# Performance work log

Hardware: AMD Instinct MI355X
Metric: run time of the kernel (lower is better)

## Reference

```python
import jax, jax.numpy as jnp
import numpy as np

EPS = 1e-12

def _l2norm(x):
    # F.normalize(p=2, dim=-1) with torch's eps clamp
    n = jnp.sqrt(jnp.sum(x * x, axis=-1, keepdims=True))
    return x / jnp.maximum(n, EPS)

def setup_inputs() -> dict:
    key = jax.random.key(0)
    k1, k2, k3, k4 = jax.random.split(key, 4)
    B, Lq, Ld, H, D = 64, 32, 256, 768, 128
    Q_hidden = jax.random.normal(k1, (B, Lq, H), dtype=jnp.float32)
    D_hidden = jax.random.normal(k2, (B, Ld, H), dtype=jnp.float32)
    W = jax.random.normal(k3, (D, H), dtype=jnp.float32) * (1.0 / np.sqrt(H))
    d_mask = jax.random.randint(k4, (B, Ld), 0, 2).astype(bool)
    d_mask = d_mask.at[:, 0].set(True)  # every doc has >=1 valid token
    return {"Q_hidden": Q_hidden, "D_hidden": D_hidden, "W": W, "d_mask": d_mask}

def reference(Q_hidden, D_hidden, W, d_mask):
    # linear projection (no bias) + L2 normalize, as in query()/doc()
    Q = _l2norm(jnp.einsum('blh,dh->bld', Q_hidden, W))       # [B,Lq,D]
    Dv = _l2norm(jnp.einsum('blh,dh->bld', D_hidden, W))      # [B,Ld,D]
    Dv = Dv * d_mask[..., None].astype(Dv.dtype)              # zero padded/skiplist tokens
    # intra-batch cosine MaxSim: sim[b,c,q,n] = Q[b,q] . D[c,n]
    sim = jnp.einsum('bqd,cnd->bcqn', Q, Dv)                  # [B,B,Lq,Ld]
    sim = jnp.where(d_mask[None, :, None, :], sim, -jnp.inf)  # mask doc tokens
    return jnp.sum(jnp.max(sim, axis=-1), axis=-1)            # [B,B]
```

## Files before the change

kernel.cpp:

```cpp
#include <hip/hip_runtime.h>
#include <hip/hip_bf16.h>
#include <math.h>

typedef __attribute__((ext_vector_type(4))) float f32x4;
typedef __attribute__((ext_vector_type(8))) short bf16x8;

#define NB    64
#define LQ    32
#define LDOC  256
#define HDIM  768
#define DDIM  128
#define NTOK_Q (NB * LQ)
#define NTOK_D (NB * LDOC)
#define NTOK   (NTOK_Q + NTOK_D)

#define WS_OFF_W    0
#define WS_OFF_MASK 196608
#define WS_OFF_QN   212992
#define WS_OFF_DN   737280

__device__ inline short f2bf(float f) {
    unsigned u = __float_as_uint(f);
    u = (u + 0x7fffu + ((u >> 16) & 1u)) >> 16;
    return (short)u;
}

__global__ void prep(const float* __restrict__ W, short* __restrict__ Wbf,
                     const unsigned char* __restrict__ mraw,
                     unsigned short* __restrict__ maskT) {
    if (blockIdx.x < 96) {
        int i = blockIdx.x * 256 + threadIdx.x;
        float4 v = *(const float4*)(W + (size_t)i * 4);
        short4 o;
        o.x = f2bf(v.x); o.y = f2bf(v.y); o.z = f2bf(v.z); o.w = f2bf(v.w);
        *(short4*)(Wbf + (size_t)i * 4) = o;
        return;
    }
    __shared__ int dword_ok_s;
    if (threadIdx.x == 0) dword_ok_s = 1;
    __syncthreads();
    const unsigned* dw = (const unsigned*)mraw;
    int ok = 1;
    for (int i = threadIdx.x; i < 4096; i += 256) {
        unsigned v = dw[i];
        if (!(v == 0u || v == 1u || v == 0x3F800000u)) ok = 0;
    }
    if (!ok) atomicAnd(&dword_ok_s, 0);
    __syncthreads();
    const int isdw = dword_ok_s;
    for (int w = threadIdx.x; w < 1024; w += 256) {
        const int c = w >> 4, lcc = w & 15;
        unsigned bits = 0;
        if (isdw) {
            for (int nt = 0; nt < 16; ++nt)
                bits |= (dw[c * 256 + nt * 16 + lcc] ? 1u : 0u) << nt;
        } else {
            for (int nt = 0; nt < 16; ++nt)
                bits |= (mraw[c * 256 + nt * 16 + lcc] ? 1u : 0u) << nt;
        }
        maskT[w] = (unsigned short)bits;
    }
}

__global__ __launch_bounds__(256)
void proj_norm(const float* __restrict__ Qh, const float* __restrict__ Dh,
               const short* __restrict__ Wbf,
               short* __restrict__ Qn, short* __restrict__ Dn) {
    const int tid  = threadIdx.x;
    const int lane = tid & 63;
    const int wave = tid >> 6;
    const int g    = lane >> 4;
    const int lc   = lane & 15;
    const int wr   = wave >> 1;
    const int wc   = wave & 1;
    const int row0 = blockIdx.x * 32;

    const float* Asrc = (row0 < NTOK_Q) ? Qh + (size_t)row0 * HDIM
                                        : Dh + (size_t)(row0 - NTOK_Q) * HDIM;

    __shared__ alignas(16) short As[2][2048];
    __shared__ alignas(16) short Bs[2][8192];
    __shared__ float norms[2][2][16];

    const int arow = tid >> 3, au = tid & 7;
    const float* aga  = Asrc + (size_t)arow * HDIM + au * 8;
    const int    adst = arow * 64 + (au ^ (arow & 7)) * 8;
    const int n0 = tid >> 3,           u0 = tid & 7;
    const int n1 = (256 + tid) >> 3,   u1 = u0;
    const int n2 = (512 + tid) >> 3,   u2 = u0;
    const int n3 = (768 + tid) >> 3,   u3 = u0;
    const short* bga0 = Wbf + (size_t)n0 * HDIM + u0 * 8;
    const short* bga1 = Wbf + (size_t)n1 * HDIM + u1 * 8;
    const short* bga2 = Wbf + (size_t)n2 * HDIM + u2 * 8;
    const short* bga3 = Wbf + (size_t)n3 * HDIM + u3 * 8;
    const int bd0 = n0 * 64 + (u0 ^ (n0 & 7)) * 8;
    const int bd1 = n1 * 64 + (u1 ^ (n1 & 7)) * 8;
    const int bd2 = n2 * 64 + (u2 ^ (n2 & 7)) * 8;
    const int bd3 = n3 * 64 + (u3 ^ (n3 & 7)) * 8;

    float4 ar0, ar1;
    bf16x8 br0, br1, br2, br3;

    auto LOADS = [&](int t) {
        ar0 = *(const float4*)(aga + t * 64);
        ar1 = *(const float4*)(aga + t * 64 + 4);
        br0 = *(const bf16x8*)(bga0 + t * 64);
        br1 = *(const bf16x8*)(bga1 + t * 64);
        br2 = *(const bf16x8*)(bga2 + t * 64);
        br3 = *(const bf16x8*)(bga3 + t * 64);
    };
    auto WRITES = [&](int buf) {
        bf16x8 av;
        av[0] = f2bf(ar0.x); av[1] = f2bf(ar0.y); av[2] = f2bf(ar0.z); av[3] = f2bf(ar0.w);
        av[4] = f2bf(ar1.x); av[5] = f2bf(ar1.y); av[6] = f2bf(ar1.z); av[7] = f2bf(ar1.w);
        *(bf16x8*)(&As[buf][adst]) = av;
        *(bf16x8*)(&Bs[buf][bd0]) = br0;
        *(bf16x8*)(&Bs[buf][bd1]) = br1;
        *(bf16x8*)(&Bs[buf][bd2]) = br2;
        *(bf16x8*)(&Bs[buf][bd3]) = br3;
    };

    f32x4 acc[4];
#pragma unroll
    for (int nt = 0; nt < 4; ++nt) acc[nt] = (f32x4){0.f, 0.f, 0.f, 0.f};

    LOADS(0);
    WRITES(0);
    __syncthreads();

    for (int t = 0; t < 12; ++t) {
        const int cur = t & 1;
        if (t < 11) LOADS(t + 1);
        __builtin_amdgcn_sched_barrier(0);

        const short* Ab = &As[cur][0];
        const short* Bb = &Bs[cur][0];
#pragma unroll
        for (int ks = 0; ks < 2; ++ks) {
            bf16x8 bfr[4];
#pragma unroll
            for (int nt = 0; nt < 4; ++nt) {
                const int nl = wc * 64 + nt * 16 + lc;
                const int c8 = (ks * 4 + g) ^ (nl & 7);
                bfr[nt] = *(const bf16x8*)(Bb + (size_t)nl * 64 + c8 * 8);
            }
            const int rl = wr * 16 + lc;
            const int ua = (ks * 4 + g) ^ (rl & 7);
            bf16x8 af = *(const bf16x8*)(Ab + (size_t)rl * 64 + ua * 8);
#pragma unroll
            for (int nt = 0; nt < 4; ++nt)
                acc[nt] = __builtin_amdgcn_mfma_f32_16x16x32_bf16(af, bfr[nt], acc[nt], 0, 0, 0);
        }
        if (t < 11) WRITES(cur ^ 1);
        __syncthreads();
    }

    float part[4];
#pragma unroll
    for (int i = 0; i < 4; ++i) {
        float s = 0.f;
#pragma unroll
        for (int nt = 0; nt < 4; ++nt) s += acc[nt][i] * acc[nt][i];
        s += __shfl_xor(s, 1);
        s += __shfl_xor(s, 2);
        s += __shfl_xor(s, 4);
        s += __shfl_xor(s, 8);
        part[i] = s;
    }
    if (lc == 0) {
#pragma unroll
        for (int i = 0; i < 4; ++i) norms[wr][wc][g * 4 + i] = part[i];
    }
    __syncthreads();

    short* Obase = (row0 < NTOK_Q) ? Qn + (size_t)row0 * DDIM
                                   : Dn + (size_t)(row0 - NTOK_Q) * DDIM;
#pragma unroll
    for (int i = 0; i < 4; ++i) {
        const int rloc = g * 4 + i;
        const float tot = norms[wr][0][rloc] + norms[wr][1][rloc];
        const float inv = 1.f / fmaxf(sqrtf(tot), 1e-12f);
        short* dst = Obase + (size_t)(wr * 16 + rloc) * DDIM + wc * 64;
#pragma unroll
        for (int nt = 0; nt < 4; ++nt)
            dst[nt * 16 + lc] = f2bf(acc[nt][i] * inv);
    }
}

__global__ __launch_bounds__(512)
void maxsim(const short* __restrict__ Qn, const short* __restrict__ Dn,
            const unsigned short* __restrict__ maskT, float* __restrict__ out) {
    const int x  = blockIdx.x & 7;
    const int m8 = (blockIdx.x >> 3) & 7;
    const int bg = blockIdx.x >> 6;
    const int c  = x * 8 + m8;

    const int tid  = threadIdx.x;
    const int wave = tid >> 6;
    const int lane = tid & 63;
    const int g = lane >> 4, lc = lane & 15;

    __shared__ alignas(16) short Ds[2][8192];

    const short* dsrc = Dn + (size_t)c * LDOC * DDIM;

    const int r0 = tid >> 4,          v0 = tid & 15;
    const int r1 = (512 + tid) >> 4,  v1 = v0;
    const int dd0 = r0 * DDIM + (v0 ^ (r0 & 15)) * 8;
    const int dd1 = r1 * DDIM + (v1 ^ (r1 & 15)) * 8;
    bf16x8 dr0, dr1;

    auto LOADS = [&](int ch) {
        dr0 = *(const bf16x8*)(dsrc + (size_t)(ch * 64 + r0) * DDIM + v0 * 8);
        dr1 = *(const bf16x8*)(dsrc + (size_t)(ch * 64 + r1) * DDIM + v1 * 8);
    };
    auto WRITES = [&](int buf) {
        *(bf16x8*)(&Ds[buf][dd0]) = dr0;
        *(bf16x8*)(&Ds[buf][dd1]) = dr1;
    };

    LOADS(0);
    WRITES(0);

    bf16x8 qf[2][4];
    const int qrow0 = bg * 256 + wave * 32;
#pragma unroll
    for (int m = 0; m < 2; ++m) {
        const short* qb = Qn + (size_t)(qrow0 + m * 16 + lc) * DDIM;
#pragma unroll
        for (int ks = 0; ks < 4; ++ks)
            qf[m][ks] = *(const bf16x8*)(qb + ks * 32 + g * 8);
    }
    const unsigned mbits = maskT[c * 16 + lc];

    __syncthreads();

    float rmax[2][4];
#pragma unroll
    for (int m = 0; m < 2; ++m)
#pragma unroll
        for (int i = 0; i < 4; ++i) rmax[m][i] = -INFINITY;

    for (int ch = 0; ch < 4; ++ch) {
        const int buf = ch & 1;
        if (ch < 3) LOADS(ch + 1);
        __builtin_amdgcn_sched_barrier(0);
        const short* Db = &Ds[buf][0];
#pragma unroll
        for (int j = 0; j < 4; ++j) {
            const int rowl = j * 16 + lc;
            bf16x8 bf[4];
#pragma unroll
            for (int ks = 0; ks < 4; ++ks) {
                const int c16 = (ks * 4 + g) ^ lc;
                bf[ks] = *(const bf16x8*)(Db + (size_t)rowl * DDIM + c16 * 8);
            }
            const bool on = (mbits >> (ch * 4 + j)) & 1;
#pragma unroll
            for (int m = 0; m < 2; ++m) {
                f32x4 acc = (f32x4){0.f, 0.f, 0.f, 0.f};
#pragma unroll
                for (int ks = 0; ks < 4; ++ks)
                    acc = __builtin_amdgcn_mfma_f32_16x16x32_bf16(qf[m][ks], bf[ks], acc, 0, 0, 0);
#pragma unroll
                for (int i = 0; i < 4; ++i)
                    rmax[m][i] = on ? fmaxf(rmax[m][i], acc[i]) : rmax[m][i];
            }
        }
        if (ch < 3) WRITES(buf ^ 1);
        __syncthreads();
    }

    float s = 0.f;
#pragma unroll
    for (int m = 0; m < 2; ++m)
#pragma unroll
        for (int i = 0; i < 4; ++i) {
            float r = rmax[m][i];
            r = fmaxf(r, __shfl_xor(r, 1));
            r = fmaxf(r, __shfl_xor(r, 2));
            r = fmaxf(r, __shfl_xor(r, 4));
            r = fmaxf(r, __shfl_xor(r, 8));
            s += r;
        }
    s += __shfl_xor(s, 16);
    s += __shfl_xor(s, 32);

    if (lane == 0) {
        const int b = bg * 8 + wave;
        out[(size_t)b * NB + c] = s;
    }
}

extern "C" void kernel_launch(void* const* d_in, const int* in_sizes, int n_in,
                              void* d_out, int out_size, void* d_ws, size_t ws_size,
                              hipStream_t stream) {
    const float* Qh = (const float*)d_in[0];
    const float* Dh = (const float*)d_in[1];
    const float* W  = (const float*)d_in[2];
    const unsigned char* dm = (const unsigned char*)d_in[3];
    float* out = (float*)d_out;
    char* ws = (char*)d_ws;

    short*          Wbf   = (short*)(ws + WS_OFF_W);
    unsigned short* maskT = (unsigned short*)(ws + WS_OFF_MASK);
    short*          Qn    = (short*)(ws + WS_OFF_QN);
    short*          Dn    = (short*)(ws + WS_OFF_DN);

    prep<<<97, 256, 0, stream>>>(W, Wbf, dm, maskT);
    proj_norm<<<NTOK / 32, 256, 0, stream>>>(Qh, Dh, Wbf, Qn, Dn);
    maxsim<<<512, 512, 0, stream>>>(Qn, Dn, maskT, out);
}
```

Before: 41.52 us.

## Load projection operands directly to registers with split-K across waves

The projection kernel stops staging A and W tiles through shared memory. Each wave now loads its MFMA fragments straight from global memory into registers with register double-buffering. Block rows drop from 32 to 16, and the K dimension is split across two wave pairs, whose partial sums are reduced through shared memory before normalization. This removes the per-step LDS writes and barriers, but W is re-read from global/L2 by every wave with less coalesced access, and twice as many blocks are launched.

```diff
diff --git a/kernel.cpp b/kernel.cpp
--- a/kernel.cpp
+++ b/kernel.cpp
@@ -69,121 +69,103 @@
     const int tid  = threadIdx.x;
     const int lane = tid & 63;
     const int wave = tid >> 6;
+    const int ch   = wave & 1;
+    const int kh   = wave >> 1;
     const int g    = lane >> 4;
     const int lc   = lane & 15;
-    const int wr   = wave >> 1;
-    const int wc   = wave & 1;
-    const int row0 = blockIdx.x * 32;
+    const int row0 = blockIdx.x * 16;
 
     const float* Asrc = (row0 < NTOK_Q) ? Qh + (size_t)row0 * HDIM
                                         : Dh + (size_t)(row0 - NTOK_Q) * HDIM;
-
-    __shared__ alignas(16) short As[2][2048];
-    __shared__ alignas(16) short Bs[2][8192];
-    __shared__ float norms[2][2][16];
-
-    const int arow = tid >> 3, au = tid & 7;
-    const float* aga  = Asrc + (size_t)arow * HDIM + au * 8;
-    const int    adst = arow * 64 + (au ^ (arow & 7)) * 8;
-    const int n0 = tid >> 3,           u0 = tid & 7;
-    const int n1 = (256 + tid) >> 3,   u1 = u0;
-    const int n2 = (512 + tid) >> 3,   u2 = u0;
-    const int n3 = (768 + tid) >> 3,   u3 = u0;
-    const short* bga0 = Wbf + (size_t)n0 * HDIM + u0 * 8;
-    const short* bga1 = Wbf + (size_t)n1 * HDIM + u1 * 8;
-    const short* bga2 = Wbf + (size_t)n2 * HDIM + u2 * 8;
-    const short* bga3 = Wbf + (size_t)n3 * HDIM + u3 * 8;
-    const int bd0 = n0 * 64 + (u0 ^ (n0 & 7)) * 8;
-    const int bd1 = n1 * 64 + (u1 ^ (n1 & 7)) * 8;
-    const int bd2 = n2 * 64 + (u2 ^ (n2 & 7)) * 8;
-    const int bd3 = n3 * 64 + (u3 ^ (n3 & 7)) * 8;
-
-    float4 ar0, ar1;
-    bf16x8 br0, br1, br2, br3;
-
-    auto LOADS = [&](int t) {
-        ar0 = *(const float4*)(aga + t * 64);
-        ar1 = *(const float4*)(aga + t * 64 + 4);
-        br0 = *(const bf16x8*)(bga0 + t * 64);
-        br1 = *(const bf16x8*)(bga1 + t * 64);
-        br2 = *(const bf16x8*)(bga2 + t * 64);
-        br3 = *(const bf16x8*)(bga3 + t * 64);
-    };
-    auto WRITES = [&](int buf) {
-        bf16x8 av;
-        av[0] = f2bf(ar0.x); av[1] = f2bf(ar0.y); av[2] = f2bf(ar0.z); av[3] = f2bf(ar0.w);
-        av[4] = f2bf(ar1.x); av[5] = f2bf(ar1.y); av[6] = f2bf(ar1.z); av[7] = f2bf(ar1.w);
-        *(bf16x8*)(&As[buf][adst]) = av;
-        *(bf16x8*)(&Bs[buf][bd0]) = br0;
-        *(bf16x8*)(&Bs[buf][bd1]) = br1;
-        *(bf16x8*)(&Bs[buf][bd2]) = br2;
-        *(bf16x8*)(&Bs[buf][bd3]) = br3;
-    };
+    const float* aptr = Asrc + (size_t)lc * HDIM + kh * 384 + g * 8;
+    const short* b0 = Wbf + (size_t)(ch * 64 +  0 + lc) * HDIM + kh * 384 + g * 8;
+    const short* b1 = Wbf + (size_t)(ch * 64 + 16 + lc) * HDIM + kh * 384 + g * 8;
+    const short* b2 = Wbf + (size_t)(ch * 64 + 32 + lc) * HDIM + kh * 384 + g * 8;
+    const short* b3 = Wbf + (size_t)(ch * 64 + 48 + lc) * HDIM + kh * 384 + g * 8;
 
     f32x4 acc[4];
 #pragma unroll
     for (int nt = 0; nt < 4; ++nt) acc[nt] = (f32x4){0.f, 0.f, 0.f, 0.f};
 
-    LOADS(0);
-    WRITES(0);
-    __syncthreads();
-
-    for (int t = 0; t < 12; ++t) {
-        const int cur = t & 1;
-        if (t < 11) LOADS(t + 1);
+    float4 sa[2][2];
+    bf16x8 sb[2][4];
+    sa[0][0] = *(const float4*)(aptr);
+    sa[0][1] = *(const float4*)(aptr + 4);
+    sb[0][0] = *(const bf16x8*)(b0);
+    sb[0][1] = *(const bf16x8*)(b1);
+    sb[0][2] = *(const bf16x8*)(b2);
+    sb[0][3] = *(const bf16x8*)(b3);
+
+#pragma unroll
+    for (int ks = 0; ks < 12; ++ks) {
+        const int cur = ks & 1, nxt = cur ^ 1;
+        if (ks < 11) {
+            const int o = (ks + 1) * 32;
+            sa[nxt][0] = *(const float4*)(aptr + o);
+            sa[nxt][1] = *(const float4*)(aptr + o + 4);
+            sb[nxt][0] = *(const bf16x8*)(b0 + o);
+            sb[nxt][1] = *(const bf16x8*)(b1 + o);
+            sb[nxt][2] = *(const bf16x8*)(b2 + o);
+            sb[nxt][3] = *(const bf16x8*)(b3 + o);
+        }
         __builtin_amdgcn_sched_barrier(0);
-
-        const short* Ab = &As[cur][0];
-        const short* Bb = &Bs[cur][0];
-#pragma unroll
-        for (int ks = 0; ks < 2; ++ks) {
-            bf16x8 bfr[4];
-#pragma unroll
-            for (int nt = 0; nt < 4; ++nt) {
-                const int nl = wc * 64 + nt * 16 + lc;
-                const int c8 = (ks * 4 + g) ^ (nl & 7);
-                bfr[nt] = *(const bf16x8*)(Bb + (size_t)nl * 64 + c8 * 8);
-            }
-            const int rl = wr * 16 + lc;
-            const int ua = (ks * 4 + g) ^ (rl & 7);
-            bf16x8 af = *(const bf16x8*)(Ab + (size_t)rl * 64 + ua * 8);
+        bf16x8 af;
+        af[0] = f2bf(sa[cur][0].x); af[1] = f2bf(sa[cur][0].y);
+        af[2] = f2bf(sa[cur][0].z); af[3] = f2bf(sa[cur][0].w);
+        af[4] = f2bf(sa[cur][1].x); af[5] = f2bf(sa[cur][1].y);
+        af[6] = f2bf(sa[cur][1].z); af[7] = f2bf(sa[cur][1].w);
+#pragma unroll
+        for (int nt = 0; nt < 4; ++nt)
+            acc[nt] = __builtin_amdgcn_mfma_f32_16x16x32_bf16(af, sb[cur][nt], acc[nt], 0, 0, 0);
+    }
+
+    __shared__ float accx[2][64][16];
+    __shared__ float norms[2][16];
+
+    if (kh == 1) {
+#pragma unroll
+        for (int nt = 0; nt < 4; ++nt)
+            *(f32x4*)&accx[ch][lane][nt * 4] = acc[nt];
+    }
+    __syncthreads();
+
+    if (kh == 0) {
+#pragma unroll
+        for (int nt = 0; nt < 4; ++nt)
+            acc[nt] += *(const f32x4*)&accx[ch][lane][nt * 4];
+
+        float part[4];
+#pragma unroll
+        for (int i = 0; i < 4; ++i) {
+            float s = 0.f;
+#pragma unroll
+            for (int nt = 0; nt < 4; ++nt) s += acc[nt][i] * acc[nt][i];
+            s += __shfl_xor(s, 1);
+            s += __shfl_xor(s, 2);
+            s += __shfl_xor(s, 4);
+            s += __shfl_xor(s, 8);
+            part[i] = s;
+        }
+        if (lc == 0) {
+#pragma unroll
+            for (int i = 0; i < 4; ++i) norms[ch][g * 4 + i] = part[i];
+        }
+    }
+    __syncthreads();
+
+    if (kh == 0) {
+        short* Obase = (row0 < NTOK_Q) ? Qn + (size_t)row0 * DDIM
+                                       : Dn + (size_t)(row0 - NTOK_Q) * DDIM;
+#pragma unroll
+        for (int i = 0; i < 4; ++i) {
+            const int rloc = g * 4 + i;
+            const float tot = norms[0][rloc] + norms[1][rloc];
+            const float inv = 1.f / fmaxf(sqrtf(tot), 1e-12f);
+            short* dst = Obase + (size_t)rloc * DDIM + ch * 64;
 #pragma unroll
             for (int nt = 0; nt < 4; ++nt)
-                acc[nt] = __builtin_amdgcn_mfma_f32_16x16x32_bf16(af, bfr[nt], acc[nt], 0, 0, 0);
-        }
-        if (t < 11) WRITES(cur ^ 1);
-        __syncthreads();
-    }
-
-    float part[4];
-#pragma unroll
-    for (int i = 0; i < 4; ++i) {
-        float s = 0.f;
-#pragma unroll
-        for (int nt = 0; nt < 4; ++nt) s += acc[nt][i] * acc[nt][i];
-        s += __shfl_xor(s, 1);
-        s += __shfl_xor(s, 2);
-        s += __shfl_xor(s, 4);
-        s += __shfl_xor(s, 8);
-        part[i] = s;
-    }
-    if (lc == 0) {
-#pragma unroll
-        for (int i = 0; i < 4; ++i) norms[wr][wc][g * 4 + i] = part[i];
-    }
-    __syncthreads();
-
-    short* Obase = (row0 < NTOK_Q) ? Qn + (size_t)row0 * DDIM
-                                   : Dn + (size_t)(row0 - NTOK_Q) * DDIM;
-#pragma unroll
-    for (int i = 0; i < 4; ++i) {
-        const int rloc = g * 4 + i;
-        const float tot = norms[wr][0][rloc] + norms[wr][1][rloc];
-        const float inv = 1.f / fmaxf(sqrtf(tot), 1e-12f);
-        short* dst = Obase + (size_t)(wr * 16 + rloc) * DDIM + wc * 64;
-#pragma unroll
-        for (int nt = 0; nt < 4; ++nt)
-            dst[nt * 16 + lc] = f2bf(acc[nt][i] * inv);
+                dst[nt * 16 + lc] = f2bf(acc[nt][i] * inv);
+        }
     }
 }
 
@@ -210,9 +192,9 @@
     const int dd1 = r1 * DDIM + (v1 ^ (r1 & 15)) * 8;
     bf16x8 dr0, dr1;
 
-    auto LOADS = [&](int ch) {
-        dr0 = *(const bf16x8*)(dsrc + (size_t)(ch * 64 + r0) * DDIM + v0 * 8);
-        dr1 = *(const bf16x8*)(dsrc + (size_t)(ch * 64 + r1) * DDIM + v1 * 8);
+    auto LOADS = [&](int chk) {
+        dr0 = *(const bf16x8*)(dsrc + (size_t)(chk * 64 + r0) * DDIM + v0 * 8);
+        dr1 = *(const bf16x8*)(dsrc + (size_t)(chk * 64 + r1) * DDIM + v1 * 8);
     };
     auto WRITES = [&](int buf) {
         *(bf16x8*)(&Ds[buf][dd0]) = dr0;
@@ -241,9 +223,9 @@
 #pragma unroll
         for (int i = 0; i < 4; ++i) rmax[m][i] = -INFINITY;
 
-    for (int ch = 0; ch < 4; ++ch) {
-        const int buf = ch & 1;
-        if (ch < 3) LOADS(ch + 1);
+    for (int chk = 0; chk < 4; ++chk) {
+        const int buf = chk & 1;
+        if (chk < 3) LOADS(chk + 1);
         __builtin_amdgcn_sched_barrier(0);
         const short* Db = &Ds[buf][0];
 #pragma unroll
@@ -255,7 +237,7 @@
                 const int c16 = (ks * 4 + g) ^ lc;
                 bf[ks] = *(const bf16x8*)(Db + (size_t)rowl * DDIM + c16 * 8);
             }
-            const bool on = (mbits >> (ch * 4 + j)) & 1;
+            const bool on = (mbits >> (chk * 4 + j)) & 1;
 #pragma unroll
             for (int m = 0; m < 2; ++m) {
                 f32x4 acc = (f32x4){0.f, 0.f, 0.f, 0.f};
@@ -267,7 +249,7 @@
                     rmax[m][i] = on ? fmaxf(rmax[m][i], acc[i]) : rmax[m][i];
             }
         }
-        if (ch < 3) WRITES(buf ^ 1);
+        if (chk < 3) WRITES(buf ^ 1);
         __syncthreads();
     }
 
@@ -308,6 +290,6 @@
     short*          Dn    = (short*)(ws + WS_OFF_DN);
 
     prep<<<97, 256, 0, stream>>>(W, Wbf, dm, maskT);
-    proj_norm<<<NTOK / 32, 256, 0, stream>>>(Qh, Dh, Wbf, Qn, Dn);
+    proj_norm<<<NTOK / 16, 256, 0, stream>>>(Qh, Dh, Wbf, Qn, Dn);
     maxsim<<<512, 512, 0, stream>>>(Qn, Dn, maskT, out);
 }
```

Result: slower. 67.97 us (+63.7%).
